# Kernel optimization log

Measured on AMD Instinct MI355X. Metric: run time of the kernel, lower is better.

## Reference

```python
import jax, jax.numpy as jnp
import numpy as np

B, N, C, L = 2, 128, 256, 3
NODE_IN, EDGE_IN = 128, 64
KN, KE = 101, 7
ALPHA = 0.2
EPS = 1e-5

def lrelu(x):
    return jax.nn.leaky_relu(x, ALPHA)

def layer_norm(x, g, b):
    mu = jnp.mean(x, axis=-1, keepdims=True)
    var = jnp.mean((x - mu) ** 2, axis=-1, keepdims=True)
    return (x - mu) / jnp.sqrt(var + EPS) * g + b

def setup_inputs() -> dict:
    key = jax.random.key(0)
    ks = jax.random.split(key, 20)
    s = 0.05
    nodes = jax.random.normal(ks[0], (B, N, NODE_IN), jnp.float32)
    edges = jax.random.normal(ks[1], (B, N, N, EDGE_IN), jnp.float32)
    m = (jax.random.uniform(ks[2], (B, N, N)) > 0.3).astype(jnp.float32)
    adj_mask = jnp.maximum(m, jnp.eye(N, dtype=jnp.float32)[None])  # guarantee non-empty rows
    return {
        'nodes': nodes, 'edges': edges, 'adj_mask': adj_mask,
        'pnW': jax.random.normal(ks[3], (C, NODE_IN)) * s, 'pnb': jnp.zeros((C,)),
        'peW': jax.random.normal(ks[4], (C, EDGE_IN)) * s, 'peb': jnp.zeros((C,)),
        'Wb': jax.random.normal(ks[5], (L, C, 3 * C)) * s,
        'Wbp': jax.random.normal(ks[6], (L, C, C)) * s,
        'Wfp': jax.random.normal(ks[7], (L, C, C)) * s,
        'ub': jax.random.normal(ks[8], (L, C)) * s,
        'Wf': jax.random.normal(ks[9], (L, C, C)) * s,
        'eln_g': jnp.ones((L, C)), 'eln_b': jnp.zeros((L, C)),
        'nln_g': jnp.ones((L, C)), 'nln_b': jnp.zeros((L, C)),
        'ncW': jax.random.normal(ks[10], (KN, C)) * s, 'ncb': jnp.zeros((KN,)),
        'ecW': jax.random.normal(ks[11], (KE, C)) * s, 'ecb': jnp.zeros((KE,)),
    }

def reference(nodes, edges, adj_mask, pnW, pnb, peW, peb, Wb, Wbp, Wfp, ub, Wf,
              eln_g, eln_b, nln_g, nln_b, ncW, ncb, ecW, ecb):
    nodes = nodes @ pnW.T + pnb          # (B,N,C)
    edges = edges @ peW.T + peb          # (B,N,N,C)
    mask3 = adj_mask[..., None]
    for l in range(Wb.shape[0]):
        Cd = nodes.shape[-1]
        Wb1, Wb2, Wb3 = Wb[l][:, :Cd], Wb[l][:, Cd:2 * Cd], Wb[l][:, 2 * Cd:]
        # W_b([f_i, edges, f_j]) without materializing the (B,N,N,3C) concat
        ai = nodes @ Wb1.T                # (B,N,C) broadcast along j
        aj = nodes @ Wb3.T                # (B,N,C) broadcast along i
        ne = lrelu(ai[:, :, None, :] + edges @ Wb2.T + aj[:, None, :, :])
        ne = ne * mask3
        new_edges = layer_norm(ne + edges, eln_g[l], eln_b[l])
        edges_in = jnp.swapaxes(new_edges, 1, 2)      # permute(0,2,1,3)
        tn = nodes @ Wfp[l].T             # shared by term_node_i / term_node_j
        st = edges_in @ Wbp[l].T + tn[:, :, None, :] + tn[:, None, :, :]
        r = lrelu(st @ ub[l])             # (B,N,N)
        r = jnp.where(adj_mask > 0, r, -jnp.inf)
        attn = jnp.nan_to_num(jax.nn.softmax(r, axis=2))
        agg = jnp.einsum('bij,bjd->bid', attn, nodes @ Wf[l].T)
        nodes = layer_norm(lrelu(agg) + nodes, nln_g[l], nln_b[l])
        edges = new_edges
    node_logits = nodes @ ncW.T + ncb
    edge_logits = edges @ ecW.T + ecb
    return (nodes, edges, node_logits, edge_logits)
```

## Files before the change

### kernel.cpp

```cpp
#include <hip/hip_runtime.h>
#include <hip/hip_bf16.h>


#define ALPHA 0.2f
#define EPS_ 1e-5f

typedef __hip_bfloat16 bf16;
typedef __bf16 bf16x8 __attribute__((ext_vector_type(8)));
typedef __bf16 bf16x4 __attribute__((ext_vector_type(4)));
typedef float floatx4 __attribute__((ext_vector_type(4)));

__device__ __forceinline__ float bf2f(bf16 x){ return __bfloat162float(x); }
__device__ __forceinline__ bf16  f2bf(float x){ return __float2bfloat16(x); }
__device__ __forceinline__ float lrelu_f(float x){ return x > 0.f ? x : ALPHA * x; }

#define T_NODES 0u
#define T_EDGES 32768u
#define T_ADJ   2129920u
#define T_PNW   2162688u
#define T_PNB   2195456u
#define T_PEW   2195712u
#define T_PEB   2212096u
#define T_WB    2212352u
#define T_WBP   2802176u
#define T_WFP   2998784u
#define T_UB    3195392u
#define T_WF    3196160u
#define T_ELNG  3392768u
#define T_ELNB  3393536u
#define T_NLNG  3394304u
#define T_NLNB  3395072u
#define T_NCW   3395840u
#define T_NCB   3421696u
#define T_ECW   3421800u
#define T_ECB   3423592u

#define O_NODES 0u
#define O_EDGES 65536u
#define O_NLOG  8454144u
#define O_ELOG  8480000u

struct SrcPtrs { const void* p[20]; };

__device__ __forceinline__ float rawld(const void* p, size_t i, bool isb){
    return isb ? bf2f(((const bf16*)p)[i]) : ((const float*)p)[i];
}

__device__ __forceinline__ bf16x8 ldfrag8(const void* p, size_t e, bool isb){
    if (isb) return *reinterpret_cast<const bf16x8*>((const bf16*)p + e);
    const float4* f = (const float4*)((const float*)p + e);
    float4 a = f[0], b = f[1];
    bf16 o[8];
    o[0]=f2bf(a.x); o[1]=f2bf(a.y); o[2]=f2bf(a.z); o[3]=f2bf(a.w);
    o[4]=f2bf(b.x); o[5]=f2bf(b.y); o[6]=f2bf(b.z); o[7]=f2bf(b.w);
    return *reinterpret_cast<bf16x8*>(o);
}

__global__ __launch_bounds__(256) void setup_k(SrcPtrs sp, bf16* __restrict__ canon,
                                               float* __restrict__ vbuf, float* __restrict__ wbuf,
                                               float* __restrict__ nodes_cur,
                                               bf16* __restrict__ rw2, bf16* __restrict__ rpe){
    const unsigned short* probe = (const unsigned short*)sp.p[12];
    const bool isb = (probe[0] == 0x3F80);
    int blk = blockIdx.x, tid = threadIdx.x;
    int wave = tid >> 6, lane = tid & 63, quad = lane >> 4, l16 = lane & 15;

    if (blk < 1024){
        const unsigned COFF[20] = {T_NODES,T_EDGES,T_ADJ,T_PNW,T_PNB,T_PEW,T_PEB,T_WB,T_WBP,T_WFP,
                                   T_UB,T_WF,T_ELNG,T_ELNB,T_NLNG,T_NLNB,T_NCW,T_NCB,T_ECW,T_ECB};
        const unsigned SZ[20]   = {32768u,2097152u,32768u,32768u,256u,16384u,256u,589824u,196608u,196608u,
                                   768u,196608u,768u,768u,768u,768u,25856u,101u,1792u,7u};
        unsigned gtid = blk*256u + tid;
        unsigned gstride = 1024u*256u;
        for (int t = 0; t < 20; ++t){
            const void* src = sp.p[t];
            unsigned coff = COFF[t], n = SZ[t];
            unsigned chunks = n >> 3;
            if (isb){
                const uint4* s4 = (const uint4*)src;
                for (unsigned idx = gtid; idx < chunks; idx += gstride)
                    *reinterpret_cast<uint4*>(canon + coff + idx*8u) = s4[idx];
            } else {
                const float4* s4 = (const float4*)src;
                for (unsigned idx = gtid; idx < chunks; idx += gstride){
                    float4 a = s4[2*idx], b = s4[2*idx+1];
                    bf16 o[8];
                    o[0]=f2bf(a.x); o[1]=f2bf(a.y); o[2]=f2bf(a.z); o[3]=f2bf(a.w);
                    o[4]=f2bf(b.x); o[5]=f2bf(b.y); o[6]=f2bf(b.z); o[7]=f2bf(b.w);
                    *reinterpret_cast<uint4*>(canon + coff + idx*8u) = *reinterpret_cast<uint4*>(o);
                }
            }
            unsigned tail = n & 7u;
            if (gtid < tail){
                unsigned li = chunks*8u + gtid;
                canon[coff + li] = isb ? ((const bf16*)src)[li] : f2bf(((const float*)src)[li]);
            }
        }
    } else if (blk < 1030){
        int q = blk - 1024;
        int l = q >> 1, m = q & 1;
        const void* W = m ? sp.p[9] : sp.p[8];
        float* out = (m ? wbuf : vbuf) + l*256;
        int c = tid;
        __shared__ float shu[256];
        shu[c] = rawld(sp.p[10], l*256 + c, isb);
        __syncthreads();
        float a0=0.f, a1=0.f, a2=0.f, a3=0.f;
        for (int cp0 = 0; cp0 < 256; cp0 += 16){
#pragma unroll
            for (int j = 0; j < 16; ++j){
                float wv = rawld(W, (size_t)l*65536u + (size_t)(cp0+j)*256u + c, isb);
                float pr = shu[cp0+j] * wv;
                if ((j & 3) == 0) a0 += pr;
                else if ((j & 3) == 1) a1 += pr;
                else if ((j & 3) == 2) a2 += pr;
                else a3 += pr;
            }
        }
        out[c] = (a0 + a1) + (a2 + a3);
    } else if (blk < 1038){
        int row0 = (blk - 1030) * 32;
        floatx4 acc[2][4] = {};
#pragma unroll
        for (int k0c = 0; k0c < 4; ++k0c){
            int k0 = k0c*32;
            bf16x8 a[2], bb[4];
#pragma unroll
            for (int mt = 0; mt < 2; ++mt)
                a[mt] = ldfrag8(sp.p[0], (size_t)(row0 + mt*16 + l16)*128u + k0 + quad*8, isb);
#pragma unroll
            for (int nt = 0; nt < 4; ++nt)
                bb[nt] = ldfrag8(sp.p[3], (size_t)(wave*64 + nt*16 + l16)*128u + k0 + quad*8, isb);
#pragma unroll
            for (int mt = 0; mt < 2; ++mt)
#pragma unroll
                for (int nt = 0; nt < 4; ++nt)
                    acc[mt][nt] = __builtin_amdgcn_mfma_f32_16x16x32_bf16(a[mt], bb[nt], acc[mt][nt], 0, 0, 0);
        }
#pragma unroll
        for (int nt = 0; nt < 4; ++nt){
            int n = wave*64 + nt*16 + l16;
            float bn = rawld(sp.p[4], n, isb);
#pragma unroll
            for (int mt = 0; mt < 2; ++mt)
#pragma unroll
                for (int reg = 0; reg < 4; ++reg){
                    int r = row0 + mt*16 + quad*4 + reg;
                    nodes_cur[r*256 + n] = acc[mt][nt][reg] + bn;
                }
        }
    } else if (blk < 1086){
        int rb = blk - 1038;
        int l = rb >> 4, n_tile = rb & 15;
        bf16* dst = rw2 + l*65536;
#pragma unroll
        for (int half = 0; half < 2; ++half){
            int slot = half*256 + tid;
            int k0c = slot >> 6, ln = slot & 63;
            int qd = ln >> 4, lw = ln & 15;
            int n = n_tile*16 + lw;
            bf16 o[8];
#pragma unroll
            for (int j = 0; j < 8; ++j){
                int k = k0c*32 + qd*8 + j;
                o[j] = f2bf(rawld(sp.p[7], (size_t)l*196608u + (size_t)n*768u + 256u + k, isb));
            }
            *reinterpret_cast<uint4*>(dst + ((k0c*16 + n_tile)*64 + ln)*8) = *reinterpret_cast<uint4*>(o);
        }
    } else {
        int n_tile = blk - 1086;
        if (tid < 128){
            int slot = tid;
            int k0c = slot >> 6, ln = slot & 63;
            int qd = ln >> 4, lw = ln & 15;
            int n = n_tile*16 + lw;
            bf16 o[8];
#pragma unroll
            for (int j = 0; j < 8; ++j){
                int k = k0c*32 + qd*8 + j;
                o[j] = f2bf(rawld(sp.p[5], (size_t)n*64u + k, isb));
            }
            *reinterpret_cast<uint4*>(rpe + ((n_tile*2 + k0c)*64 + ln)*8) = *reinterpret_cast<uint4*>(o);
        }
    }
}

__global__ __launch_bounds__(256) void node_linears_k(
        const float* __restrict__ nodes_cur, const bf16* __restrict__ Wb_l,
        const bf16* __restrict__ Wf_l, const float* __restrict__ w_l,
        float* __restrict__ ai, float* __restrict__ aj,
        float* __restrict__ nf, float* __restrict__ s){
    int row = blockIdx.x;
    int c = threadIdx.x;
    __shared__ float x[256];
    __shared__ float red[4];
    x[c] = nodes_cur[row*256 + c];
    __syncthreads();
    float xs = x[c] * w_l[c];
    for (int off = 32; off; off >>= 1) xs += __shfl_xor(xs, off, 64);
    if ((c & 63) == 0) red[c >> 6] = xs;
    const bf16x8* w1 = reinterpret_cast<const bf16x8*>(Wb_l + (size_t)c*768);
    const bf16x8* w3 = reinterpret_cast<const bf16x8*>(Wb_l + (size_t)c*768 + 512);
    const bf16x8* wf = reinterpret_cast<const bf16x8*>(Wf_l + (size_t)c*256);
    float a1 = 0.f, a3 = 0.f, f = 0.f;
#pragma unroll 4
    for (int ch = 0; ch < 32; ++ch){
        bf16x8 v1 = w1[ch], v3 = w3[ch], vf = wf[ch];
#pragma unroll
        for (int j = 0; j < 8; ++j){
            float xv = x[ch*8 + j];
            a1 += xv * (float)v1[j];
            a3 += xv * (float)v3[j];
            f  += xv * (float)vf[j];
        }
    }
    ai[row*256 + c] = a1;
    aj[row*256 + c] = a3;
    nf[row*256 + c] = f;
    __syncthreads();
    if (c == 0) s[row] = red[0] + red[1] + red[2] + red[3];
}

__global__ __launch_bounds__(256, 3) void edge_update2_k(
        bf16* __restrict__ Ebuf, const bf16* __restrict__ rw2_l,
        const float* __restrict__ ai, const float* __restrict__ aj,
        const bf16* __restrict__ adj, const bf16* __restrict__ g, const bf16* __restrict__ bta,
        const float* __restrict__ v, float* __restrict__ rbuf,
        int isfinal, const bf16* __restrict__ ecW, const bf16* __restrict__ ecb,
        void* __restrict__ dout, const unsigned short* __restrict__ probe,
        int isfirst, const bf16* __restrict__ eIn, const bf16* __restrict__ rpe,
        const bf16* __restrict__ peb){
    int row0 = blockIdx.x * 32;
    int b = row0 >> 14, i = (row0 >> 7) & 127, j0 = row0 & 127;
    int tid = threadIdx.x;
    int wave = tid >> 6, lane = tid & 63, quad = lane >> 4, l16 = lane & 15;

    __shared__ bf16  shA[32*264];
    __shared__ float sh_ai[256];
    __shared__ float sh_v[256];
    __shared__ float sh_g[256];
    __shared__ float sh_bt[256];
    __shared__ float sh_w7[7][256];
    __shared__ float smS[4][32];
    __shared__ float smQ[4][32];
    __shared__ float dvp[4][32];
    __shared__ float lgp[4][32][7];

    float maskv[2];
    float4 ajp[2][4];
#pragma unroll
    for (int rf = 0; rf < 2; ++rf){
        int j = j0 + rf*16 + l16;
        maskv[rf] = bf2f(adj[(b*128 + i)*128 + j]);
        const float* ajrow = aj + (size_t)(b*128 + j)*256 + wave*64;
#pragma unroll
        for (int mt = 0; mt < 4; ++mt)
            ajp[rf][mt] = *reinterpret_cast<const float4*>(ajrow + mt*16 + quad*4);
    }

    sh_ai[tid] = ai[(b*128 + i)*256 + tid];
    sh_v[tid]  = v[tid];
    sh_g[tid]  = bf2f(g[tid]);
    sh_bt[tid] = bf2f(bta[tid]);
    if (isfirst){
        floatx4 pacc[2][4] = {};
#pragma unroll
        for (int k0c = 0; k0c < 2; ++k0c){
            int k0 = k0c*32;
            bf16x8 a[2], bb[4];
#pragma unroll
            for (int mt = 0; mt < 2; ++mt)
                a[mt] = *reinterpret_cast<const bf16x8*>(eIn + (size_t)(row0 + mt*16 + l16)*64 + k0 + quad*8);
#pragma unroll
            for (int nt = 0; nt < 4; ++nt)
                bb[nt] = *reinterpret_cast<const bf16x8*>(rpe + ((size_t)((wave*4 + nt)*2 + k0c)*64 + lane)*8);
#pragma unroll
            for (int mt = 0; mt < 2; ++mt)
#pragma unroll
                for (int nt = 0; nt < 4; ++nt)
                    pacc[mt][nt] = __builtin_amdgcn_mfma_f32_16x16x32_bf16(a[mt], bb[nt], pacc[mt][nt], 0, 0, 0);
        }
#pragma unroll
        for (int nt = 0; nt < 4; ++nt){
            int col = wave*64 + nt*16 + l16;
            float bbv = bf2f(peb[col]);
#pragma unroll
            for (int mt = 0; mt < 2; ++mt)
#pragma unroll
                for (int reg = 0; reg < 4; ++reg)
                    shA[(mt*16 + quad*4 + reg)*264 + col] = f2bf(pacc[mt][nt][reg] + bbv);
        }
    } else {
#pragma unroll
        for (int it = 0; it < 4; ++it){
            int idx = it*256 + tid;
            int r = idx >> 5, c8 = idx & 31;
            bf16x8 vA = *reinterpret_cast<const bf16x8*>(Ebuf + (size_t)(row0 + r)*256 + c8*8);
            *reinterpret_cast<bf16x8*>(&shA[r*264 + c8*8]) = vA;
        }
    }
    if (isfinal){
        for (int idx = tid; idx < 7*256; idx += 256)
            sh_w7[idx >> 8][idx & 255] = bf2f(ecW[idx]);
    }
    __syncthreads();

    floatx4 acc[4][2] = {};
    {
        const bf16* shb = &shA[l16*264];
        for (int k0c = 0; k0c < 8; ++k0c){
            bf16x8 bfr[2];
#pragma unroll
            for (int rf = 0; rf < 2; ++rf)
                bfr[rf] = *reinterpret_cast<const bf16x8*>(shb + rf*16*264 + k0c*32 + quad*8);
#pragma unroll
            for (int mt = 0; mt < 4; ++mt){
                bf16x8 afrag = *reinterpret_cast<const bf16x8*>(
                    rw2_l + ((size_t)(k0c*16 + wave*4 + mt)*64 + lane)*8);
#pragma unroll
                for (int rf = 0; rf < 2; ++rf)
                    acc[mt][rf] = __builtin_amdgcn_mfma_f32_16x16x32_bf16(afrag, bfr[rf], acc[mt][rf], 0, 0, 0);
            }
        }
    }

    const bool isb = (probe[0] == 0x3F80);
#pragma unroll
    for (int rf = 0; rf < 2; ++rf){
        int rl = rf*16 + l16;
        float sm = 0.f, q = 0.f;
#pragma unroll
        for (int mt = 0; mt < 4; ++mt){
            int c0 = wave*64 + mt*16 + quad*4;
            float4 aiv = *reinterpret_cast<const float4*>(sh_ai + c0);
            bf16x4 ev  = *reinterpret_cast<const bf16x4*>(&shA[rl*264 + c0]);
#pragma unroll
            for (int reg = 0; reg < 4; ++reg){
                float y = acc[mt][rf][reg] + ((const float*)&aiv)[reg] + ((const float*)&ajp[rf][mt])[reg];
                float x = lrelu_f(y) * maskv[rf] + (float)ev[reg];
                acc[mt][rf][reg] = x;
                sm += x; q += x*x;
            }
        }
        sm += __shfl_xor(sm, 16, 64); sm += __shfl_xor(sm, 32, 64);
        q  += __shfl_xor(q, 16, 64);  q  += __shfl_xor(q, 32, 64);
        if (quad == 0){ smS[wave][rl] = sm; smQ[wave][rl] = q; }
    }
    __syncthreads();

#pragma unroll
    for (int rf = 0; rf < 2; ++rf){
        int rl = rf*16 + l16;
        float ts = smS[0][rl] + smS[1][rl] + smS[2][rl] + smS[3][rl];
        float tq = smQ[0][rl] + smQ[1][rl] + smQ[2][rl] + smQ[3][rl];
        float mu  = ts * (1.f/256.f);
        float var = tq * (1.f/256.f) - mu*mu;
        float rstd = rsqrtf(var + EPS_);
        float dv = 0.f;
        float lg[7] = {0.f,0.f,0.f,0.f,0.f,0.f,0.f};
#pragma unroll
        for (int mt = 0; mt < 4; ++mt){
            int c0 = wave*64 + mt*16 + quad*4;
            float4 gv = *reinterpret_cast<const float4*>(sh_g + c0);
            float4 bv = *reinterpret_cast<const float4*>(sh_bt + c0);
            float4 vv = *reinterpret_cast<const float4*>(sh_v + c0);
            bf16x4 ob;
#pragma unroll
            for (int reg = 0; reg < 4; ++reg){
                float xo = (acc[mt][rf][reg] - mu) * rstd * ((const float*)&gv)[reg] + ((const float*)&bv)[reg];
                ob[reg] = f2bf(xo);
                dv += xo * ((const float*)&vv)[reg];
                if (isfinal){
#pragma unroll
                    for (int k = 0; k < 7; ++k) lg[k] += xo * sh_w7[k][c0 + reg];
                }
            }
            *reinterpret_cast<bf16x4*>(&shA[rl*264 + c0]) = ob;
        }
        dv += __shfl_xor(dv, 16, 64); dv += __shfl_xor(dv, 32, 64);
        if (quad == 0) dvp[wave][rl] = dv;
        if (isfinal){
#pragma unroll
            for (int k = 0; k < 7; ++k){
                lg[k] += __shfl_xor(lg[k], 16, 64);
                lg[k] += __shfl_xor(lg[k], 32, 64);
            }
            if (quad == 0){
#pragma unroll
                for (int k = 0; k < 7; ++k) lgp[wave][rl][k] = lg[k];
            }
        }
    }
    __syncthreads();

    if (!isfinal){
#pragma unroll
        for (int it = 0; it < 4; ++it){
            int idx = it*256 + tid;
            int r = idx >> 5, c8 = idx & 31;
            *reinterpret_cast<bf16x8*>(Ebuf + (size_t)(row0 + r)*256 + c8*8) =
                *reinterpret_cast<const bf16x8*>(&shA[r*264 + c8*8]);
        }
    } else if (isb){
#pragma unroll
        for (int it = 0; it < 4; ++it){
            int idx = it*256 + tid;
            int r = idx >> 5, c8 = idx & 31;
            *reinterpret_cast<bf16x8*>((bf16*)dout + O_EDGES + (size_t)(row0 + r)*256 + c8*8) =
                *reinterpret_cast<const bf16x8*>(&shA[r*264 + c8*8]);
        }
    } else {
#pragma unroll
        for (int it = 0; it < 4; ++it){
            int idx = it*256 + tid;
            int r = idx >> 5, c8 = idx & 31;
            bf16x8 vA = *reinterpret_cast<const bf16x8*>(&shA[r*264 + c8*8]);
            float4 f0, f1;
            f0.x = (float)vA[0]; f0.y = (float)vA[1]; f0.z = (float)vA[2]; f0.w = (float)vA[3];
            f1.x = (float)vA[4]; f1.y = (float)vA[5]; f1.z = (float)vA[6]; f1.w = (float)vA[7];
            float* op = (float*)dout + O_EDGES + (size_t)(row0 + r)*256 + c8*8;
            *reinterpret_cast<float4*>(op)     = f0;
            *reinterpret_cast<float4*>(op + 4) = f1;
        }
    }

    if (wave == 0 && quad == 0){
#pragma unroll
        for (int rf = 0; rf < 2; ++rf){
            int rl = rf*16 + l16;
            int j  = j0 + rl;
            int grow = row0 + rl;
            float d = dvp[0][rl] + dvp[1][rl] + dvp[2][rl] + dvp[3][rl];
            rbuf[(b*128 + j)*128 + i] = d;
            if (isfinal){
#pragma unroll
                for (int k = 0; k < 7; ++k){
                    float val = lgp[0][rl][k] + lgp[1][rl][k] + lgp[2][rl][k] + lgp[3][rl][k] + bf2f(ecb[k]);
                    if (isb) ((bf16*)dout)[O_ELOG + (size_t)grow*7 + k] = f2bf(val);
                    else     ((float*)dout)[O_ELOG + (size_t)grow*7 + k] = val;
                }
            }
        }
    }
}

__global__ __launch_bounds__(256) void node_update_k(
        const float* __restrict__ rbuf, const float* __restrict__ s_in, const bf16* __restrict__ adj,
        const float* __restrict__ nf_in, float* __restrict__ nodes_cur,
        const bf16* __restrict__ g, const bf16* __restrict__ bta,
        int isfinal,
        const bf16* __restrict__ Wb_nx, const bf16* __restrict__ Wf_nx, const float* __restrict__ w_nx,
        float* __restrict__ ai_o, float* __restrict__ aj_o, float* __restrict__ nf_o, float* __restrict__ s_o,
        const bf16* __restrict__ ncW, const bf16* __restrict__ ncb,
        void* __restrict__ dout, const unsigned short* __restrict__ probe){
    int row = blockIdx.x;
    int b = row >> 7;
    int tid = threadIdx.x;
    int wave = tid >> 6, lane = tid & 63;
    __shared__ float attn[128];
    __shared__ float shr[16];
    __shared__ float shfx[256];

    float rv = -__builtin_inff();
    if (tid < 128){
        float t = rbuf[row*128 + tid] + s_in[row] + s_in[b*128 + tid];
        t = lrelu_f(t);
        rv = (bf2f(adj[row*128 + tid]) > 0.f) ? t : -__builtin_inff();
    }
    float m = rv;
    for (int off = 32; off; off >>= 1) m = fmaxf(m, __shfl_xor(m, off, 64));
    if (lane == 0) shr[wave] = m;
    __syncthreads();
    float mx = fmaxf(fmaxf(shr[0], shr[1]), fmaxf(shr[2], shr[3]));
    float e = (tid < 128 && rv > -__builtin_inff()) ? expf(rv - mx) : 0.f;
    if (tid < 128) attn[tid] = e;
    float se = e;
    for (int off = 32; off; off >>= 1) se += __shfl_xor(se, off, 64);
    if (lane == 0) shr[4 + wave] = se;
    __syncthreads();
    float inv = 1.f / (shr[4] + shr[5] + shr[6] + shr[7]);

    int c = tid;
    const float* nfb = nf_in + (size_t)b*32768 + c;
    float g0 = 0.f, g1 = 0.f, g2 = 0.f, g3 = 0.f;
    float g4 = 0.f, g5 = 0.f, g6 = 0.f, g7 = 0.f;
    for (int jj = 0; jj < 128; jj += 8){
        g0 += attn[jj]   * nfb[(size_t)jj*256];
        g1 += attn[jj+1] * nfb[(size_t)(jj+1)*256];
        g2 += attn[jj+2] * nfb[(size_t)(jj+2)*256];
        g3 += attn[jj+3] * nfb[(size_t)(jj+3)*256];
        g4 += attn[jj+4] * nfb[(size_t)(jj+4)*256];
        g5 += attn[jj+5] * nfb[(size_t)(jj+5)*256];
        g6 += attn[jj+6] * nfb[(size_t)(jj+6)*256];
        g7 += attn[jj+7] * nfb[(size_t)(jj+7)*256];
    }
    float agg = (((g0 + g1) + (g2 + g3)) + ((g4 + g5) + (g6 + g7))) * inv;
    float x = lrelu_f(agg) + nodes_cur[row*256 + c];
    float xs = x, xq = x*x;
    for (int off = 32; off; off >>= 1){ xs += __shfl_xor(xs, off, 64); xq += __shfl_xor(xq, off, 64); }
    if (lane == 0){ shr[8 + wave] = xs; shr[12 + wave] = xq; }
    __syncthreads();
    float sum = shr[8] + shr[9] + shr[10] + shr[11];
    float sq  = shr[12] + shr[13] + shr[14] + shr[15];
    float mu  = sum * (1.f/256.f);
    float var = sq * (1.f/256.f) - mu*mu;
    float rstd = rsqrtf(var + EPS_);
    float out = (x - mu) * rstd * bf2f(g[c]) + bf2f(bta[c]);
    nodes_cur[row*256 + c] = out;
    shfx[c] = out;
    __syncthreads();

    if (!isfinal){
        float ws2 = out * w_nx[c];
        for (int off = 32; off; off >>= 1) ws2 += __shfl_xor(ws2, off, 64);
        if (lane == 0) shr[wave] = ws2;
        const bf16x8* w1 = reinterpret_cast<const bf16x8*>(Wb_nx + (size_t)c*768);
        const bf16x8* w3 = reinterpret_cast<const bf16x8*>(Wb_nx + (size_t)c*768 + 512);
        const bf16x8* wf = reinterpret_cast<const bf16x8*>(Wf_nx + (size_t)c*256);
        float a1 = 0.f, a3 = 0.f, f = 0.f;
#pragma unroll 4
        for (int ch = 0; ch < 32; ++ch){
            bf16x8 v1 = w1[ch], v3 = w3[ch], vf = wf[ch];
#pragma unroll
            for (int j = 0; j < 8; ++j){
                float xv = shfx[ch*8 + j];
                a1 += xv * (float)v1[j];
                a3 += xv * (float)v3[j];
                f  += xv * (float)vf[j];
            }
        }
        ai_o[row*256 + c] = a1;
        aj_o[row*256 + c] = a3;
        nf_o[row*256 + c] = f;
        __syncthreads();
        if (c == 0) s_o[row] = shr[0] + shr[1] + shr[2] + shr[3];
    } else {
        const bool isb = (probe[0] == 0x3F80);
        if (isb) ((bf16*)dout)[O_NODES + row*256 + c] = f2bf(out);
        else     ((float*)dout)[O_NODES + row*256 + c] = out;
        if (tid < 101){
            const bf16x8* wr = reinterpret_cast<const bf16x8*>(ncW + (size_t)tid*256);
            float acc = bf2f(ncb[tid]);
#pragma unroll 4
            for (int ch = 0; ch < 32; ++ch){
                bf16x8 wv = wr[ch];
#pragma unroll
                for (int j = 0; j < 8; ++j) acc += shfx[ch*8 + j] * (float)wv[j];
            }
            if (isb) ((bf16*)dout)[O_NLOG + row*101 + tid] = f2bf(acc);
            else     ((float*)dout)[O_NLOG + row*101 + tid] = acc;
        }
    }
}

extern "C" void kernel_launch(void* const* d_in, const int* in_sizes, int n_in,
                              void* d_out, int out_size, void* d_ws, size_t ws_size,
                              hipStream_t stream){
    (void)in_sizes; (void)n_in; (void)out_size; (void)ws_size;

    SrcPtrs sp;
    for (int i = 0; i < 20; ++i) sp.p[i] = d_in[i];
    const unsigned short* probe = (const unsigned short*)d_in[12];

    bf16* canon = (bf16*)d_ws;
    char* ws2 = (char*)d_ws + 6847488;
    bf16* Ebuf = (bf16*)ws2;
    float* f = (float*)(ws2 + 16777216);
    float* ai    = f;
    float* aj    = f + 65536;
    float* nfA   = f + 131072;
    float* nfB   = f + 196608;
    float* sA    = f + 262144;
    float* sB    = f + 262400;
    float* rbuf  = f + 262656;
    float* vbuf  = f + 295424;
    float* wbuf  = f + 296192;
    float* nodes_cur = f + 296960;
    bf16* rw2 = (bf16*)(f + 362496);
    bf16* rpe = rw2 + 196608;

    const bf16* c_edges = canon + T_EDGES;
    const bf16* c_adj   = canon + T_ADJ;
    const bf16* c_peb   = canon + T_PEB;
    const bf16* c_Wb    = canon + T_WB;
    const bf16* c_Wf    = canon + T_WF;
    const bf16* c_elng  = canon + T_ELNG;
    const bf16* c_elnb  = canon + T_ELNB;
    const bf16* c_nlng  = canon + T_NLNG;
    const bf16* c_nlnb  = canon + T_NLNB;
    const bf16* c_ncW   = canon + T_NCW;
    const bf16* c_ncb   = canon + T_NCB;
    const bf16* c_ecW   = canon + T_ECW;
    const bf16* c_ecb   = canon + T_ECB;

    setup_k<<<dim3(1102), dim3(256), 0, stream>>>(sp, canon, vbuf, wbuf, nodes_cur, rw2, rpe);
    node_linears_k<<<dim3(256), dim3(256), 0, stream>>>(
        nodes_cur, c_Wb, c_Wf, wbuf, ai, aj, nfA, sA);

    for (int l = 0; l < 3; ++l){
        int fin = (l == 2);
        int fst = (l == 0);
        float* nf_in = (l & 1) ? nfB : nfA;
        float* nf_out = (l & 1) ? nfA : nfB;
        float* s_in  = (l & 1) ? sB : sA;
        float* s_out = (l & 1) ? sA : sB;
        edge_update2_k<<<dim3(1024), dim3(256), 0, stream>>>(
            Ebuf, rw2 + l*65536, ai, aj, c_adj,
            c_elng + l*256, c_elnb + l*256, vbuf + l*256, rbuf,
            fin, c_ecW, c_ecb, d_out, probe,
            fst, c_edges, rpe, c_peb);
        node_update_k <<<dim3(256), dim3(256), 0, stream>>>(
            rbuf, s_in, c_adj, nf_in, nodes_cur, c_nlng + l*256, c_nlnb + l*256,
            fin,
            c_Wb + (size_t)(l+1)*196608, c_Wf + (size_t)(l+1)*65536, wbuf + (l+1)*256,
            ai, aj, nf_out, s_out,
            c_ncW, c_ncb, d_out, probe);
    }
}
```

Measured before the change: 263.6 us.

## Split node GEMV reductions across two thread halves; trim edge kernel LDS for occupancy

The node linear and node update kernels now launch 512 threads per row. The K dimension of each GEMV and of the attention aggregation is split into two halves, and the partial sums are combined through shared memory. The edge update kernel drops its per-block LDS copies of gamma, beta and v in favour of direct global loads, keeps the final classifier weights in LDS as bf16, raises the min-blocks launch bound from 3 to 4 and fully unrolls the MFMA k-loop. The goal is more parallelism in the small node kernels and higher occupancy in the dominant edge kernel, at the cost of extra syncs and possible register spills under the tighter bound.

```diff
diff --git a/kernel.cpp b/kernel.cpp
--- a/kernel.cpp
+++ b/kernel.cpp
@@ -185,43 +185,53 @@
     }
 }
 
-__global__ __launch_bounds__(256) void node_linears_k(
+__global__ __launch_bounds__(512) void node_linears_k(
         const float* __restrict__ nodes_cur, const bf16* __restrict__ Wb_l,
         const bf16* __restrict__ Wf_l, const float* __restrict__ w_l,
         float* __restrict__ ai, float* __restrict__ aj,
         float* __restrict__ nf, float* __restrict__ s){
     int row = blockIdx.x;
-    int c = threadIdx.x;
+    int tid = threadIdx.x;
+    int wave = tid >> 6, lane = tid & 63;
+    int c = tid & 255, kh = tid >> 8;
     __shared__ float x[256];
-    __shared__ float red[4];
-    x[c] = nodes_cur[row*256 + c];
-    __syncthreads();
-    float xs = x[c] * w_l[c];
-    for (int off = 32; off; off >>= 1) xs += __shfl_xor(xs, off, 64);
-    if ((c & 63) == 0) red[c >> 6] = xs;
-    const bf16x8* w1 = reinterpret_cast<const bf16x8*>(Wb_l + (size_t)c*768);
-    const bf16x8* w3 = reinterpret_cast<const bf16x8*>(Wb_l + (size_t)c*768 + 512);
-    const bf16x8* wf = reinterpret_cast<const bf16x8*>(Wf_l + (size_t)c*256);
+    __shared__ float red[8];
+    __shared__ float pp1[2][256], pp3[2][256], ppf[2][256];
+
+    if (tid < 256) x[c] = nodes_cur[row*256 + c];
+    __syncthreads();
+    if (tid < 256){
+        float xs = x[c] * w_l[c];
+        for (int off = 32; off; off >>= 1) xs += __shfl_xor(xs, off, 64);
+        if (lane == 0) red[wave] = xs;
+    }
+    const bf16x8* w1 = reinterpret_cast<const bf16x8*>(Wb_l + (size_t)c*768 + kh*128);
+    const bf16x8* w3 = reinterpret_cast<const bf16x8*>(Wb_l + (size_t)c*768 + 512 + kh*128);
+    const bf16x8* wf = reinterpret_cast<const bf16x8*>(Wf_l + (size_t)c*256 + kh*128);
+    const float* xb = x + kh*128;
     float a1 = 0.f, a3 = 0.f, f = 0.f;
 #pragma unroll 4
-    for (int ch = 0; ch < 32; ++ch){
+    for (int ch = 0; ch < 16; ++ch){
         bf16x8 v1 = w1[ch], v3 = w3[ch], vf = wf[ch];
 #pragma unroll
         for (int j = 0; j < 8; ++j){
-            float xv = x[ch*8 + j];
+            float xv = xb[ch*8 + j];
             a1 += xv * (float)v1[j];
             a3 += xv * (float)v3[j];
             f  += xv * (float)vf[j];
         }
     }
-    ai[row*256 + c] = a1;
-    aj[row*256 + c] = a3;
-    nf[row*256 + c] = f;
-    __syncthreads();
-    if (c == 0) s[row] = red[0] + red[1] + red[2] + red[3];
+    pp1[kh][c] = a1; pp3[kh][c] = a3; ppf[kh][c] = f;
+    __syncthreads();
+    if (tid < 256){
+        ai[row*256 + c] = pp1[0][c] + pp1[1][c];
+        aj[row*256 + c] = pp3[0][c] + pp3[1][c];
+        nf[row*256 + c] = ppf[0][c] + ppf[1][c];
+    }
+    if (tid == 0) s[row] = red[0] + red[1] + red[2] + red[3];
 }
 
-__global__ __launch_bounds__(256, 3) void edge_update2_k(
+__global__ __launch_bounds__(256, 4) void edge_update2_k(
         bf16* __restrict__ Ebuf, const bf16* __restrict__ rw2_l,
         const float* __restrict__ ai, const float* __restrict__ aj,
         const bf16* __restrict__ adj, const bf16* __restrict__ g, const bf16* __restrict__ bta,
@@ -237,10 +247,7 @@
 
     __shared__ bf16  shA[32*264];
     __shared__ float sh_ai[256];
-    __shared__ float sh_v[256];
-    __shared__ float sh_g[256];
-    __shared__ float sh_bt[256];
-    __shared__ float sh_w7[7][256];
+    __shared__ bf16  sh_w7b[7][256];
     __shared__ float smS[4][32];
     __shared__ float smQ[4][32];
     __shared__ float dvp[4][32];
@@ -259,9 +266,6 @@
     }
 
     sh_ai[tid] = ai[(b*128 + i)*256 + tid];
-    sh_v[tid]  = v[tid];
-    sh_g[tid]  = bf2f(g[tid]);
-    sh_bt[tid] = bf2f(bta[tid]);
     if (isfirst){
         floatx4 pacc[2][4] = {};
 #pragma unroll
@@ -301,13 +305,14 @@
     }
     if (isfinal){
         for (int idx = tid; idx < 7*256; idx += 256)
-            sh_w7[idx >> 8][idx & 255] = bf2f(ecW[idx]);
+            sh_w7b[idx >> 8][idx & 255] = ecW[idx];
     }
     __syncthreads();
 
     floatx4 acc[4][2] = {};
     {
         const bf16* shb = &shA[l16*264];
+#pragma unroll
         for (int k0c = 0; k0c < 8; ++k0c){
             bf16x8 bfr[2];
 #pragma unroll
@@ -361,18 +366,18 @@
 #pragma unroll
         for (int mt = 0; mt < 4; ++mt){
             int c0 = wave*64 + mt*16 + quad*4;
-            float4 gv = *reinterpret_cast<const float4*>(sh_g + c0);
-            float4 bv = *reinterpret_cast<const float4*>(sh_bt + c0);
-            float4 vv = *reinterpret_cast<const float4*>(sh_v + c0);
+            bf16x4 gv4 = *reinterpret_cast<const bf16x4*>(g + c0);
+            bf16x4 bv4 = *reinterpret_cast<const bf16x4*>(bta + c0);
+            float4 vv  = *reinterpret_cast<const float4*>(v + c0);
             bf16x4 ob;
 #pragma unroll
             for (int reg = 0; reg < 4; ++reg){
-                float xo = (acc[mt][rf][reg] - mu) * rstd * ((const float*)&gv)[reg] + ((const float*)&bv)[reg];
+                float xo = (acc[mt][rf][reg] - mu) * rstd * (float)gv4[reg] + (float)bv4[reg];
                 ob[reg] = f2bf(xo);
                 dv += xo * ((const float*)&vv)[reg];
                 if (isfinal){
 #pragma unroll
-                    for (int k = 0; k < 7; ++k) lg[k] += xo * sh_w7[k][c0 + reg];
+                    for (int k = 0; k < 7; ++k) lg[k] += xo * (float)sh_w7b[k][c0 + reg];
                 }
             }
             *reinterpret_cast<bf16x4*>(&shA[rl*264 + c0]) = ob;
@@ -444,7 +449,7 @@
     }
 }
 
-__global__ __launch_bounds__(256) void node_update_k(
+__global__ __launch_bounds__(512) void node_update_k(
         const float* __restrict__ rbuf, const float* __restrict__ s_in, const bf16* __restrict__ adj,
         const float* __restrict__ nf_in, float* __restrict__ nodes_cur,
         const bf16* __restrict__ g, const bf16* __restrict__ bta,
@@ -457,9 +462,12 @@
     int b = row >> 7;
     int tid = threadIdx.x;
     int wave = tid >> 6, lane = tid & 63;
+    int c = tid & 255, kh = tid >> 8;
     __shared__ float attn[128];
-    __shared__ float shr[16];
+    __shared__ float shr[32];
     __shared__ float shfx[256];
+    __shared__ float aggp[2][256];
+    __shared__ float pp1[2][256], pp3[2][256], ppf[2][256];
 
     float rv = -__builtin_inff();
     if (tid < 128){
@@ -469,86 +477,111 @@
     }
     float m = rv;
     for (int off = 32; off; off >>= 1) m = fmaxf(m, __shfl_xor(m, off, 64));
-    if (lane == 0) shr[wave] = m;
-    __syncthreads();
-    float mx = fmaxf(fmaxf(shr[0], shr[1]), fmaxf(shr[2], shr[3]));
+    if (lane == 0 && wave < 2) shr[wave] = m;
+    __syncthreads();
+    float mx = fmaxf(shr[0], shr[1]);
     float e = (tid < 128 && rv > -__builtin_inff()) ? expf(rv - mx) : 0.f;
     if (tid < 128) attn[tid] = e;
     float se = e;
     for (int off = 32; off; off >>= 1) se += __shfl_xor(se, off, 64);
-    if (lane == 0) shr[4 + wave] = se;
-    __syncthreads();
-    float inv = 1.f / (shr[4] + shr[5] + shr[6] + shr[7]);
-
-    int c = tid;
-    const float* nfb = nf_in + (size_t)b*32768 + c;
-    float g0 = 0.f, g1 = 0.f, g2 = 0.f, g3 = 0.f;
-    float g4 = 0.f, g5 = 0.f, g6 = 0.f, g7 = 0.f;
-    for (int jj = 0; jj < 128; jj += 8){
-        g0 += attn[jj]   * nfb[(size_t)jj*256];
-        g1 += attn[jj+1] * nfb[(size_t)(jj+1)*256];
-        g2 += attn[jj+2] * nfb[(size_t)(jj+2)*256];
-        g3 += attn[jj+3] * nfb[(size_t)(jj+3)*256];
-        g4 += attn[jj+4] * nfb[(size_t)(jj+4)*256];
-        g5 += attn[jj+5] * nfb[(size_t)(jj+5)*256];
-        g6 += attn[jj+6] * nfb[(size_t)(jj+6)*256];
-        g7 += attn[jj+7] * nfb[(size_t)(jj+7)*256];
-    }
-    float agg = (((g0 + g1) + (g2 + g3)) + ((g4 + g5) + (g6 + g7))) * inv;
-    float x = lrelu_f(agg) + nodes_cur[row*256 + c];
-    float xs = x, xq = x*x;
-    for (int off = 32; off; off >>= 1){ xs += __shfl_xor(xs, off, 64); xq += __shfl_xor(xq, off, 64); }
-    if (lane == 0){ shr[8 + wave] = xs; shr[12 + wave] = xq; }
-    __syncthreads();
-    float sum = shr[8] + shr[9] + shr[10] + shr[11];
-    float sq  = shr[12] + shr[13] + shr[14] + shr[15];
-    float mu  = sum * (1.f/256.f);
-    float var = sq * (1.f/256.f) - mu*mu;
-    float rstd = rsqrtf(var + EPS_);
-    float out = (x - mu) * rstd * bf2f(g[c]) + bf2f(bta[c]);
-    nodes_cur[row*256 + c] = out;
-    shfx[c] = out;
+    if (lane == 0 && wave < 2) shr[2 + wave] = se;
+    __syncthreads();
+    float inv = 1.f / (shr[2] + shr[3]);
+
+    {
+        const float* nfb = nf_in + (size_t)b*32768 + c;
+        int jb = kh*64;
+        float g0 = 0.f, g1 = 0.f, g2 = 0.f, g3 = 0.f;
+        float g4 = 0.f, g5 = 0.f, g6 = 0.f, g7 = 0.f;
+        for (int jj = jb; jj < jb + 64; jj += 8){
+            g0 += attn[jj]   * nfb[(size_t)jj*256];
+            g1 += attn[jj+1] * nfb[(size_t)(jj+1)*256];
+            g2 += attn[jj+2] * nfb[(size_t)(jj+2)*256];
+            g3 += attn[jj+3] * nfb[(size_t)(jj+3)*256];
+            g4 += attn[jj+4] * nfb[(size_t)(jj+4)*256];
+            g5 += attn[jj+5] * nfb[(size_t)(jj+5)*256];
+            g6 += attn[jj+6] * nfb[(size_t)(jj+6)*256];
+            g7 += attn[jj+7] * nfb[(size_t)(jj+7)*256];
+        }
+        aggp[kh][c] = ((g0 + g1) + (g2 + g3)) + ((g4 + g5) + (g6 + g7));
+    }
+    __syncthreads();
+
+    float x = 0.f;
+    if (tid < 256){
+        float agg = (aggp[0][c] + aggp[1][c]) * inv;
+        x = lrelu_f(agg) + nodes_cur[row*256 + c];
+        float xs = x, xq = x*x;
+        for (int off = 32; off; off >>= 1){ xs += __shfl_xor(xs, off, 64); xq += __shfl_xor(xq, off, 64); }
+        if (lane == 0){ shr[8 + wave] = xs; shr[16 + wave] = xq; }
+    }
+    __syncthreads();
+    float out = 0.f;
+    if (tid < 256){
+        float sum = shr[8] + shr[9] + shr[10] + shr[11];
+        float sq  = shr[16] + shr[17] + shr[18] + shr[19];
+        float mu  = sum * (1.f/256.f);
+        float var = sq * (1.f/256.f) - mu*mu;
+        float rstd = rsqrtf(var + EPS_);
+        out = (x - mu) * rstd * bf2f(g[c]) + bf2f(bta[c]);
+        nodes_cur[row*256 + c] = out;
+        shfx[c] = out;
+        if (!isfinal){
+            float ws2 = out * w_nx[c];
+            for (int off = 32; off; off >>= 1) ws2 += __shfl_xor(ws2, off, 64);
+            if (lane == 0) shr[24 + wave] = ws2;
+        }
+    }
     __syncthreads();
 
     if (!isfinal){
-        float ws2 = out * w_nx[c];
-        for (int off = 32; off; off >>= 1) ws2 += __shfl_xor(ws2, off, 64);
-        if (lane == 0) shr[wave] = ws2;
-        const bf16x8* w1 = reinterpret_cast<const bf16x8*>(Wb_nx + (size_t)c*768);
-        const bf16x8* w3 = reinterpret_cast<const bf16x8*>(Wb_nx + (size_t)c*768 + 512);
-        const bf16x8* wf = reinterpret_cast<const bf16x8*>(Wf_nx + (size_t)c*256);
+        const bf16x8* w1 = reinterpret_cast<const bf16x8*>(Wb_nx + (size_t)c*768 + kh*128);
+        const bf16x8* w3 = reinterpret_cast<const bf16x8*>(Wb_nx + (size_t)c*768 + 512 + kh*128);
+        const bf16x8* wf = reinterpret_cast<const bf16x8*>(Wf_nx + (size_t)c*256 + kh*128);
+        const float* xb = shfx + kh*128;
         float a1 = 0.f, a3 = 0.f, f = 0.f;
 #pragma unroll 4
-        for (int ch = 0; ch < 32; ++ch){
+        for (int ch = 0; ch < 16; ++ch){
             bf16x8 v1 = w1[ch], v3 = w3[ch], vf = wf[ch];
 #pragma unroll
             for (int j = 0; j < 8; ++j){
-                float xv = shfx[ch*8 + j];
+                float xv = xb[ch*8 + j];
                 a1 += xv * (float)v1[j];
                 a3 += xv * (float)v3[j];
                 f  += xv * (float)vf[j];
             }
         }
-        ai_o[row*256 + c] = a1;
-        aj_o[row*256 + c] = a3;
-        nf_o[row*256 + c] = f;
+        pp1[kh][c] = a1; pp3[kh][c] = a3; ppf[kh][c] = f;
         __syncthreads();
-        if (c == 0) s_o[row] = shr[0] + shr[1] + shr[2] + shr[3];
+        if (tid < 256){
+            ai_o[row*256 + c] = pp1[0][c] + pp1[1][c];
+            aj_o[row*256 + c] = pp3[0][c] + pp3[1][c];
+            nf_o[row*256 + c] = ppf[0][c] + ppf[1][c];
+        }
+        if (tid == 0) s_o[row] = shr[24] + shr[25] + shr[26] + shr[27];
     } else {
         const bool isb = (probe[0] == 0x3F80);
-        if (isb) ((bf16*)dout)[O_NODES + row*256 + c] = f2bf(out);
-        else     ((float*)dout)[O_NODES + row*256 + c] = out;
+        if (tid < 256){
+            if (isb) ((bf16*)dout)[O_NODES + row*256 + c] = f2bf(out);
+            else     ((float*)dout)[O_NODES + row*256 + c] = out;
+        }
+        if (c < 101){
+            const bf16x8* wr = reinterpret_cast<const bf16x8*>(ncW + (size_t)c*256 + kh*128);
+            const float* xb = shfx + kh*128;
+            float acc = 0.f;
+#pragma unroll 4
+            for (int ch = 0; ch < 16; ++ch){
+                bf16x8 wv = wr[ch];
+#pragma unroll
+                for (int j = 0; j < 8; ++j) acc += xb[ch*8 + j] * (float)wv[j];
+            }
+            pp1[kh][c] = acc;
+        }
+        __syncthreads();
         if (tid < 101){
-            const bf16x8* wr = reinterpret_cast<const bf16x8*>(ncW + (size_t)tid*256);
-            float acc = bf2f(ncb[tid]);
-#pragma unroll 4
-            for (int ch = 0; ch < 32; ++ch){
-                bf16x8 wv = wr[ch];
-#pragma unroll
-                for (int j = 0; j < 8; ++j) acc += shfx[ch*8 + j] * (float)wv[j];
-            }
-            if (isb) ((bf16*)dout)[O_NLOG + row*101 + tid] = f2bf(acc);
-            else     ((float*)dout)[O_NLOG + row*101 + tid] = acc;
+            float val = pp1[0][tid] + pp1[1][tid] + bf2f(ncb[tid]);
+            if (isb) ((bf16*)dout)[O_NLOG + row*101 + tid] = f2bf(val);
+            else     ((float*)dout)[O_NLOG + row*101 + tid] = val;
         }
     }
 }
@@ -594,7 +627,7 @@
     const bf16* c_ecb   = canon + T_ECB;
 
     setup_k<<<dim3(1102), dim3(256), 0, stream>>>(sp, canon, vbuf, wbuf, nodes_cur, rw2, rpe);
-    node_linears_k<<<dim3(256), dim3(256), 0, stream>>>(
+    node_linears_k<<<dim3(256), dim3(512), 0, stream>>>(
         nodes_cur, c_Wb, c_Wf, wbuf, ai, aj, nfA, sA);
 
     for (int l = 0; l < 3; ++l){
@@ -609,7 +642,7 @@
             c_elng + l*256, c_elnb + l*256, vbuf + l*256, rbuf,
             fin, c_ecW, c_ecb, d_out, probe,
             fst, c_edges, rpe, c_peb);
-        node_update_k <<<dim3(256), dim3(256), 0, stream>>>(
+        node_update_k <<<dim3(256), dim3(512), 0, stream>>>(
             rbuf, s_in, c_adj, nf_in, nodes_cur, c_nlng + l*256, c_nlnb + l*256,
             fin,
             c_Wb + (size_t)(l+1)*196608, c_Wf + (size_t)(l+1)*65536, wbuf + (l+1)*256,
```

Result: faster. 256.1 us (-2.8%).
